# Performance work log

Measured on AMD Instinct MI355X. Metric: run time of the kernel, lower is better.

Reference implementation:

```python
import jax, jax.numpy as jnp
import numpy as np

NEG_INF = -1000000000.0

def setup_inputs() -> dict:
    key = jax.random.key(0)
    k1, k2, k3, k4 = jax.random.split(key, 4)
    N, F_in, F_out, H = 4096, 256, 64, 4
    x = jax.random.normal(k1, (N, F_in), dtype=jnp.float32)
    adj = jax.random.randint(k2, (N, N), 0, 2, dtype=jnp.int32)
    W = jax.random.normal(k3, (H, F_in, F_out), dtype=jnp.float32) * 0.05
    a = jax.random.normal(k4, (H, 2 * F_out, 1), dtype=jnp.float32) * 0.05
    return {"x": x, "adj": adj, "W": W, "a": a}

def reference(x, adj, W, a):
    # x: [N, F_in], adj: [N, N] int, W: [H, F_in, F_out], a: [H, 2*F_out, 1]
    H, F_in, F_out = W.shape
    N = x.shape[0]
    h = jnp.einsum('nf,hfo->hno', x, W)              # [H, N, F_out]
    a1 = a[:, :F_out, 0]                             # [H, F_out] (dot with h_i part of concat)
    a2 = a[:, F_out:, 0]                             # [H, F_out] (dot with h_j part)
    f1 = jnp.einsum('hno,ho->hn', h, a1)             # [H, N]
    f2 = jnp.einsum('hno,ho->hn', h, a2)             # [H, N]
    e = f1[:, :, None] + f2[:, None, :]              # [H, N, N] == dot(concat(h_i,h_j), a)
    e = jnp.where(e >= 0, e, 0.2 * e)                # leaky_relu, slope 0.2
    mask = (adj == 0).astype(jnp.float32) * NEG_INF  # [N, N]
    alpha = jax.nn.softmax(e + mask[None], axis=-1)  # [H, N, N]
    # dropout deterministic (training=False) -> identity
    out = jnp.einsum('hij,hjo->hio', alpha, h)       # [H, N, F_out]
    # concat=True: concat heads along feature dim
    return jnp.transpose(out, (1, 0, 2)).reshape(N, H * F_out)
```

## Files before the change

kernel.cpp:

```cpp
#include <hip/hip_runtime.h>
#include <hip/hip_bf16.h>
#include <stdint.h>

#define LOG2E 1.4426950408889634f

typedef __attribute__((ext_vector_type(4))) float f4;
typedef __attribute__((ext_vector_type(4))) int   i4;
typedef __attribute__((ext_vector_type(8))) short s8;
typedef __attribute__((ext_vector_type(4))) short s4;

#if defined(__has_builtin)
# if __has_builtin(__builtin_amdgcn_exp2f)
#  define EXP2F(x) __builtin_amdgcn_exp2f(x)
# else
#  define EXP2F(x) exp2f(x)
# endif
#else
# define EXP2F(x) exp2f(x)
#endif

static __device__ __forceinline__ uint32_t fbits(float f) {
  union { float f; uint32_t u; } c; c.f = f; return c.u;
}
static __device__ __forceinline__ float ubits(uint32_t u) {
  union { uint32_t u; float f; } c; c.u = u; return c.f;
}
static __device__ __forceinline__ uint16_t bf16_rne(float f) {
  uint32_t b = fbits(f);
  b += 0x7FFFu + ((b >> 16) & 1u);
  return (uint16_t)(b >> 16);
}
static __device__ __forceinline__ float bf2f(uint16_t u) {
  return ubits(((uint32_t)u) << 16);
}
static __device__ __forceinline__ uint32_t fkey(float f) {
  uint32_t u = fbits(f);
  return (u >> 31) ? ~u : (u | 0x80000000u);
}
static __device__ __forceinline__ float unkey(uint32_t k) {
  return ubits((k & 0x80000000u) ? (k ^ 0x80000000u) : ~k);
}

__global__ __launch_bounds__(256) void k_prep_wt(const float* __restrict__ W,
                                                 uint16_t* __restrict__ WT,
                                                 uint32_t* __restrict__ f2mkey) {
  if (blockIdx.x == 0 && threadIdx.x < 4) f2mkey[threadIdx.x] = 0u;
  int idx = (blockIdx.x * 256 + threadIdx.x) * 4;
  f4 w = *(const f4*)(W + idx);
  int h = idx >> 14;
  int k = (idx >> 6) & 255;
  int o = idx & 63;
  uint16_t* base = WT + ((h << 6) + o) * 256 + k;
  base[0]   = bf16_rne(w.x);
  base[256] = bf16_rne(w.y);
  base[512] = bf16_rne(w.z);
  base[768] = bf16_rne(w.w);
}

__global__ __launch_bounds__(256) void k_gemm_h(
    const float* __restrict__ x, const uint16_t* __restrict__ WT,
    const float* __restrict__ a,
    uint16_t* __restrict__ hTf, float* __restrict__ f1, float* __restrict__ f2,
    uint32_t* __restrict__ f2mkey) {
  const int N = 4096, K = 256;
  __shared__ uint16_t xs[16][264];
  int t = threadIdx.x;
  int i0 = blockIdx.x * 16;
  {
    int r = t >> 4, c = (t & 15) << 4;
    const float* src = x + (i0 + r) * K + c;
    union { uint16_t u[16]; s8 v[2]; } tmp;
    #pragma unroll
    for (int i = 0; i < 16; i += 4) {
      f4 v = *(const f4*)(src + i);
      tmp.u[i+0] = bf16_rne(v.x); tmp.u[i+1] = bf16_rne(v.y);
      tmp.u[i+2] = bf16_rne(v.z); tmp.u[i+3] = bf16_rne(v.w);
    }
    *(s8*)&xs[r][c]     = tmp.v[0];
    *(s8*)&xs[r][c + 8] = tmp.v[1];
  }
  __syncthreads();
  int wave = t >> 6, lane = t & 63, lr = lane & 15, lc = lane >> 4;
  f4 acc[4];
  #pragma unroll
  for (int cg = 0; cg < 4; ++cg) acc[cg] = (f4){0.f, 0.f, 0.f, 0.f};
  #pragma unroll
  for (int ks = 0; ks < 8; ++ks) {
    s8 af = *(const s8*)&xs[lr][ks * 32 + lc * 8];
    #pragma unroll
    for (int cg = 0; cg < 4; ++cg) {
      s8 bf = *(const s8*)(WT + ((wave << 6) + (cg << 4) + lr) * 256 + ks * 32 + lc * 8);
      acc[cg] = __builtin_amdgcn_mfma_f32_16x16x32_bf16(af, bf, acc[cg], 0, 0, 0);
    }
  }
  float p1[4] = {0, 0, 0, 0}, p2[4] = {0, 0, 0, 0};
  #pragma unroll
  for (int cg = 0; cg < 4; ++cg) {
    float a1v = a[wave * 128 + (cg << 4) + lr];
    float a2v = a[wave * 128 + 64 + (cg << 4) + lr];
    #pragma unroll
    for (int q = 0; q < 4; ++q) {
      p1[q] = fmaf(acc[cg][q], a1v, p1[q]);
      p2[q] = fmaf(acc[cg][q], a2v, p2[q]);
    }
  }
  #pragma unroll
  for (int m = 1; m <= 8; m <<= 1) {
    #pragma unroll
    for (int q = 0; q < 4; ++q) {
      p1[q] += __shfl_xor(p1[q], m, 64);
      p2[q] += __shfl_xor(p2[q], m, 64);
    }
  }
  if (lr == 0) {
    #pragma unroll
    for (int q = 0; q < 4; ++q) {
      f1[wave * N + i0 + (lc << 2) + q] = p1[q];
      f2[wave * N + i0 + (lc << 2) + q] = p2[q];
    }
  }
  float wm = fmaxf(fmaxf(p2[0], p2[1]), fmaxf(p2[2], p2[3]));
  wm = fmaxf(wm, __shfl_xor(wm, 16, 64));
  wm = fmaxf(wm, __shfl_xor(wm, 32, 64));
  if (lane == 0) atomicMax(&f2mkey[wave], fkey(wm));
  int b0 = (i0 & 31) + (lc << 2);
  int hi = b0 >> 3, e0 = b0 & 7;
  size_t cbase = ((size_t)(wave * 32 + (i0 >> 7)) * 4 + ((i0 >> 5) & 3)) << 2;
  #pragma unroll
  for (int cg = 0; cg < 4; ++cg) {
    union { uint16_t u[4]; s4 v; } h4;
    #pragma unroll
    for (int q = 0; q < 4; ++q) h4.u[q] = bf16_rne(acc[cg][q]);
    *(s4*)(hTf + ((cbase + cg) << 9) + ((hi << 4) + lr) * 8 + e0) = h4.v;
  }
}

__global__ __launch_bounds__(256, 4) void k_attn(
    const int* __restrict__ adj, const float* __restrict__ f1,
    const float* __restrict__ f2, const uint32_t* __restrict__ f2mkey,
    const uint16_t* __restrict__ hTf,
    uint16_t* __restrict__ Op, float* __restrict__ lp, int NP) {
  const int N = 4096;
  __shared__ int adjs[2][32][128];
  int p = blockIdx.x % NP;
  int rb = blockIdx.x / NP;
  int i0 = rb << 5;
  int jcount = N / NP, jbase = p * jcount, ntiles = jcount >> 7;
  int t = threadIdx.x, wave = t >> 6, lane = t & 63, lr = lane & 15, lc = lane >> 4;

  float fm = unkey(f2mkey[wave]);
  float d1[2], d2[2];
  #pragma unroll
  for (int g = 0; g < 2; ++g) {
    float f1v = f1[wave * N + i0 + (g << 4) + lr];
    float s = f1v + fm;
    float M = fmaxf(s, 0.2f * s);
    d1[g] = fmaf(f1v, LOG2E, -M * LOG2E);
    d2[g] = fmaf(f1v, 0.2f * LOG2E, -M * LOG2E);
  }
  f4 acc[2][4], accl[2];
  #pragma unroll
  for (int g = 0; g < 2; ++g) {
    accl[g] = (f4){0.f, 0.f, 0.f, 0.f};
    #pragma unroll
    for (int cg = 0; cg < 4; ++cg) acc[g][cg] = (f4){0.f, 0.f, 0.f, 0.f};
  }
  const s8 ones = {0x3F80, 0x3F80, 0x3F80, 0x3F80, 0x3F80, 0x3F80, 0x3F80, 0x3F80};

  int rloc = (wave << 3) + (lane >> 5);
  int chb = lane & 31;
  const int* gbase = adj + (size_t)(i0 + rloc) * N + jbase;

  #define STAGE(TILE, BUF)                                                    \
    {                                                                         \
      int jc_ = (TILE) << 7;                                                  \
      _Pragma("unroll")                                                       \
      for (int pair = 0; pair < 4; ++pair) {                                  \
        int row_ = rloc + (pair << 1);                                        \
        int ch_ = chb ^ (row_ & 7);           \
        const int* gp_ = gbase + (size_t)(pair << 1) * N + jc_ + (ch_ << 2);  \
        __builtin_amdgcn_global_load_lds(                                     \
            (const __attribute__((address_space(1))) void*)gp_,               \
            (__attribute__((address_space(3))) void*)                         \
                &adjs[BUF][(wave << 3) + (pair << 1)][0],                     \
            16, 0, 0);                                                        \
      }                                                                       \
    }

  const float* f2b = f2 + wave * N + jbase + (lc << 3);
  const uint16_t* hTfb = hTf + (((size_t)(wave * 32) + (jbase >> 7)) << 13) + lane * 8;

  STAGE(0, 0);
  __syncthreads();

  for (int tile = 0;; ++tile) {
    int cur = tile & 1;
    if (tile + 1 < ntiles) STAGE(tile + 1, cur ^ 1);
    const uint16_t* hTft = hTfb + ((size_t)tile << 13);
    #pragma unroll
    for (int ks = 0; ks < 4; ++ks) {
      f4 f2v0 = *(const f4*)(f2b + (tile << 7) + (ks << 5));
      f4 f2v1 = *(const f4*)(f2b + (tile << 7) + (ks << 5) + 4);
      s8 bf[4];
      #pragma unroll
      for (int cg = 0; cg < 4; ++cg)
        bf[cg] = *(const s8*)(hTft + (((ks << 2) + cg) << 9));
      #pragma unroll
      for (int g = 0; g < 2; ++g) {
        const i4* rowp = (const i4*)&adjs[cur][(g << 4) + lr][0];
        int X = (ks << 3) + (lc << 1), s7 = lr & 7;
        i4 a0 = rowp[X ^ s7];
        i4 a1 = rowp[(X + 1) ^ s7];
        uint32_t eb[8];
        #pragma unroll
        for (int e = 0; e < 8; ++e) {
          float f2e = (e < 4) ? f2v0[e] : f2v1[e - 4];
          int   ai  = (e < 4) ? a0[e]   : a1[e - 4];
          float arg = fmaxf(fmaf(f2e, LOG2E, d1[g]),
                            fmaf(f2e, 0.2f * LOG2E, d2[g]));
          eb[e] = (fbits(EXP2F(arg)) & (uint32_t)(-ai)) + 0x8000u;
        }
        union { uint32_t u[4]; s8 v; } af;
        #pragma unroll
        for (int i2 = 0; i2 < 4; ++i2)
          af.u[i2] = __builtin_amdgcn_perm(eb[2 * i2 + 1], eb[2 * i2], 0x07060302u);
        #pragma unroll
        for (int cg = 0; cg < 4; ++cg)
          acc[g][cg] = __builtin_amdgcn_mfma_f32_16x16x32_bf16(af.v, bf[cg],
                                                               acc[g][cg], 0, 0, 0);
        accl[g] = __builtin_amdgcn_mfma_f32_16x16x32_bf16(af.v, ones, accl[g], 0, 0, 0);
      }
    }
    if (tile + 1 >= ntiles) break;
    __syncthreads();
  }
  #undef STAGE

  uint16_t* ob = Op + (size_t)((p << 2) + wave) * N * 64 + (size_t)i0 * 64;
  #pragma unroll
  for (int g = 0; g < 2; ++g) {
    #pragma unroll
    for (int cg = 0; cg < 4; ++cg) {
      #pragma unroll
      for (int q = 0; q < 4; ++q)
        ob[((g << 4) + (lc << 2) + q) * 64 + (cg << 4) + lr] = bf16_rne(acc[g][cg][q]);
    }
    if (lr == 0) {
      #pragma unroll
      for (int q = 0; q < 4; ++q)
        lp[(size_t)((p << 2) + wave) * N + i0 + (g << 4) + (lc << 2) + q] = accl[g][q];
    }
  }
}

__global__ __launch_bounds__(256) void k_combine(
    const uint16_t* __restrict__ Op, const float* __restrict__ lp,
    float* __restrict__ out, int NP) {
  int idx = blockIdx.x * 256 + threadIdx.x;
  int n = idx >> 5;
  int c8 = (idx & 31) << 3;
  int h = c8 >> 6, o = c8 & 63;
  float s[8] = {0, 0, 0, 0, 0, 0, 0, 0};
  float ls = 0.f;
  for (int p = 0; p < NP; ++p) {
    size_t base = (size_t)((p << 2) + h) * 4096 + n;
    s8 v = *(const s8*)(Op + base * 64 + o);
    #pragma unroll
    for (int k = 0; k < 8; ++k) s[k] += bf2f((uint16_t)v[k]);
    ls += lp[base];
  }
  float inv = (ls > 0.f) ? 1.0f / ls : 0.f;
  f4 r0 = {s[0] * inv, s[1] * inv, s[2] * inv, s[3] * inv};
  f4 r1 = {s[4] * inv, s[5] * inv, s[6] * inv, s[7] * inv};
  float* dst = out + (size_t)n * 256 + c8;
  *(f4*)dst = r0;
  *(f4*)(dst + 4) = r1;
}

extern "C" void kernel_launch(void* const* d_in, const int* in_sizes, int n_in,
                              void* d_out, int out_size, void* d_ws, size_t ws_size,
                              hipStream_t stream) {
  (void)in_sizes; (void)n_in; (void)out_size;
  const float* x   = (const float*)d_in[0];
  const int*   adj = (const int*)d_in[1];
  const float* W   = (const float*)d_in[2];
  const float* a   = (const float*)d_in[3];
  float* out = (float*)d_out;
  char* ws = (char*)d_ws;

  size_t oWT = 0;
  size_t oHT = oWT + 131072;
  size_t oF1 = oHT + 2097152;
  size_t oF2 = oF1 + 65536;
  size_t oFM = oF2 + 65536;
  size_t oOP = (oFM + 16 + 255) & ~(size_t)255;

  int NP = 8;
  while (NP > 1 && oOP + (size_t)NP * (2097152 + 65536) > ws_size) NP >>= 1;
  size_t oLP = oOP + (size_t)NP * 2097152;

  uint16_t* WT   = (uint16_t*)(ws + oWT);
  uint16_t* hTf  = (uint16_t*)(ws + oHT);
  float*    f1   = (float*)(ws + oF1);
  float*    f2   = (float*)(ws + oF2);
  uint32_t* f2mk = (uint32_t*)(ws + oFM);
  uint16_t* Op   = (uint16_t*)(ws + oOP);
  float*    lp   = (float*)(ws + oLP);

  k_prep_wt<<<64, 256, 0, stream>>>(W, WT, f2mk);
  k_gemm_h<<<256, 256, 0, stream>>>(x, WT, a, hTf, f1, f2, f2mk);
  k_attn<<<128 * NP, 256, 0, stream>>>(adj, f1, f2, f2mk, hTf, Op, lp, NP);
  k_combine<<<512, 256, 0, stream>>>(Op, lp, out, NP);
}
```

Before: 62.90 us.

## Factor softmax exponent into per-row and per-column exp products in attention

Replaces the per-element exp2 of the leaky-relu score with a product of precomputed per-row factors (exp of f1 terms) and per-column factors (exp of f2 terms, staged in LDS), selecting the branch by comparing the column factor against a per-row threshold. The row-sum is accumulated in VALU from the masked values instead of an extra MFMA against a ones vector. The split count is fixed to 16 with smaller 32-column adjacency tiles, and occupancy is raised to 5 blocks. This removes transcendental work from the inner loop. In exchange it can lose precision or overflow because of the exp products, and it drops the workspace-size fallback.

Result: slower. 104.5 us (+66.2%).

```diff
diff --git a/kernel.cpp b/kernel.cpp
--- a/kernel.cpp
+++ b/kernel.cpp
@@ -2,7 +2,8 @@
 #include <hip/hip_bf16.h>
 #include <stdint.h>
 
-#define LOG2E 1.4426950408889634f
+#define LOG2E  1.4426950408889634f
+#define LOG2E5 0.28853900817779268f
 
 typedef __attribute__((ext_vector_type(4))) float f4;
 typedef __attribute__((ext_vector_type(4))) int   i4;
@@ -135,101 +136,106 @@
   }
 }
 
-__global__ __launch_bounds__(256, 4) void k_attn(
+__global__ __launch_bounds__(256, 5) void k_attn(
     const int* __restrict__ adj, const float* __restrict__ f1,
     const float* __restrict__ f2, const uint32_t* __restrict__ f2mkey,
     const uint16_t* __restrict__ hTf,
-    uint16_t* __restrict__ Op, float* __restrict__ lp, int NP) {
+    uint16_t* __restrict__ Op, float* __restrict__ lp) {
   const int N = 4096;
-  __shared__ int adjs[2][32][128];
-  int p = blockIdx.x % NP;
-  int rb = blockIdx.x / NP;
+  __shared__ int   adjs[2][32][32];
+  __shared__ float E1s[4][256];
+  __shared__ float E2s[4][256];
+  int p  = blockIdx.x & 15;
+  int rb = blockIdx.x >> 4;
   int i0 = rb << 5;
-  int jcount = N / NP, jbase = p * jcount, ntiles = jcount >> 7;
+  int jbase = p << 8;
+  const int ntiles = 8;
   int t = threadIdx.x, wave = t >> 6, lane = t & 63, lr = lane & 15, lc = lane >> 4;
 
   float fm = unkey(f2mkey[wave]);
-  float d1[2], d2[2];
+  float a1f[2], a2f[2], Ti[2], lsum[2] = {0.f, 0.f};
   #pragma unroll
   for (int g = 0; g < 2; ++g) {
     float f1v = f1[wave * N + i0 + (g << 4) + lr];
     float s = f1v + fm;
     float M = fmaxf(s, 0.2f * s);
-    d1[g] = fmaf(f1v, LOG2E, -M * LOG2E);
-    d2[g] = fmaf(f1v, 0.2f * LOG2E, -M * LOG2E);
-  }
-  f4 acc[2][4], accl[2];
-  #pragma unroll
-  for (int g = 0; g < 2; ++g) {
-    accl[g] = (f4){0.f, 0.f, 0.f, 0.f};
+    a1f[g] = EXP2F((f1v - M) * LOG2E);
+    a2f[g] = EXP2F(fmaf(f1v, LOG2E5, -M * LOG2E));
+    Ti[g]  = EXP2F(-f1v * LOG2E);
+  }
+  {
+    int j0 = lane << 2;
+    f4 fv = *(const f4*)(f2 + wave * N + jbase + j0);
+    f4 e1, e2;
+    #pragma unroll
+    for (int k = 0; k < 4; ++k) {
+      e1[k] = EXP2F(fv[k] * LOG2E);
+      e2[k] = EXP2F(fv[k] * LOG2E5);
+    }
+    *(f4*)&E1s[wave][j0] = e1;
+    *(f4*)&E2s[wave][j0] = e2;
+  }
+
+  f4 acc[2][4];
+  #pragma unroll
+  for (int g = 0; g < 2; ++g)
     #pragma unroll
     for (int cg = 0; cg < 4; ++cg) acc[g][cg] = (f4){0.f, 0.f, 0.f, 0.f};
-  }
-  const s8 ones = {0x3F80, 0x3F80, 0x3F80, 0x3F80, 0x3F80, 0x3F80, 0x3F80, 0x3F80};
-
-  int rloc = (wave << 3) + (lane >> 5);
-  int chb = lane & 31;
-  const int* gbase = adj + (size_t)(i0 + rloc) * N + jbase;
-
-  #define STAGE(TILE, BUF)                                                    \
-    {                                                                         \
-      int jc_ = (TILE) << 7;                                                  \
-      _Pragma("unroll")                                                       \
-      for (int pair = 0; pair < 4; ++pair) {                                  \
-        int row_ = rloc + (pair << 1);                                        \
-        int ch_ = chb ^ (row_ & 7);           \
-        const int* gp_ = gbase + (size_t)(pair << 1) * N + jc_ + (ch_ << 2);  \
-        __builtin_amdgcn_global_load_lds(                                     \
-            (const __attribute__((address_space(1))) void*)gp_,               \
-            (__attribute__((address_space(3))) void*)                         \
-                &adjs[BUF][(wave << 3) + (pair << 1)][0],                     \
-            16, 0, 0);                                                        \
-      }                                                                       \
-    }
-
-  const float* f2b = f2 + wave * N + jbase + (lc << 3);
-  const uint16_t* hTfb = hTf + (((size_t)(wave * 32) + (jbase >> 7)) << 13) + lane * 8;
+
+  int srow  = lane >> 3;
+  int sslot = (lane & 7) ^ srow;
+  const int* gbase = adj + (size_t)(i0 + (wave << 3) + srow) * N + jbase + (sslot << 2);
+
+  #define STAGE(TILE, BUF)                                                  \
+    __builtin_amdgcn_global_load_lds(                                       \
+        (const __attribute__((address_space(1))) void*)(gbase + ((TILE) << 5)), \
+        (__attribute__((address_space(3))) void*)&adjs[BUF][wave << 3][0],  \
+        16, 0, 0);
 
   STAGE(0, 0);
   __syncthreads();
+
+  const uint16_t* hTfb = hTf + ((size_t)(wave * 512 + p * 32) << 9) + lane * 8;
 
   for (int tile = 0;; ++tile) {
     int cur = tile & 1;
     if (tile + 1 < ntiles) STAGE(tile + 1, cur ^ 1);
-    const uint16_t* hTft = hTfb + ((size_t)tile << 13);
-    #pragma unroll
-    for (int ks = 0; ks < 4; ++ks) {
-      f4 f2v0 = *(const f4*)(f2b + (tile << 7) + (ks << 5));
-      f4 f2v1 = *(const f4*)(f2b + (tile << 7) + (ks << 5) + 4);
-      s8 bf[4];
+    const uint16_t* hTft = hTfb + ((size_t)tile << 11);
+    s8 bf0 = *(const s8*)(hTft);
+    s8 bf1 = *(const s8*)(hTft + 512);
+    s8 bf2v = *(const s8*)(hTft + 1024);
+    s8 bf3 = *(const s8*)(hTft + 1536);
+    int jo = (tile << 5) + (lc << 3);
+    f4 E1a = *(const f4*)&E1s[wave][jo];
+    f4 E1b = *(const f4*)&E1s[wave][jo + 4];
+    f4 E2a = *(const f4*)&E2s[wave][jo];
+    f4 E2b = *(const f4*)&E2s[wave][jo + 4];
+    #pragma unroll
+    for (int g = 0; g < 2; ++g) {
+      const i4* rowp = (const i4*)&adjs[cur][(g << 4) + lr][0];
+      int sw = lr & 7;
+      i4 a0 = rowp[(lc << 1) ^ sw];
+      i4 a1v = rowp[((lc << 1) + 1) ^ sw];
+      uint32_t eb[8];
       #pragma unroll
-      for (int cg = 0; cg < 4; ++cg)
-        bf[cg] = *(const s8*)(hTft + (((ks << 2) + cg) << 9));
+      for (int e = 0; e < 8; ++e) {
+        float e1 = (e < 4) ? E1a[e] : E1b[e - 4];
+        float e2 = (e < 4) ? E2a[e] : E2b[e - 4];
+        int   ai = (e < 4) ? a0[e]  : a1v[e - 4];
+        bool  c  = e1 >= Ti[g];
+        float pf = (c ? a1f[g] : a2f[g]) * (c ? e1 : e2);
+        uint32_t mb = fbits(pf) & (uint32_t)(-ai);
+        lsum[g] += ubits(mb);
+        eb[e] = mb + 0x8000u;
+      }
+      union { uint32_t u[4]; s8 v; } af;
       #pragma unroll
-      for (int g = 0; g < 2; ++g) {
-        const i4* rowp = (const i4*)&adjs[cur][(g << 4) + lr][0];
-        int X = (ks << 3) + (lc << 1), s7 = lr & 7;
-        i4 a0 = rowp[X ^ s7];
-        i4 a1 = rowp[(X + 1) ^ s7];
-        uint32_t eb[8];
-        #pragma unroll
-        for (int e = 0; e < 8; ++e) {
-          float f2e = (e < 4) ? f2v0[e] : f2v1[e - 4];
-          int   ai  = (e < 4) ? a0[e]   : a1[e - 4];
-          float arg = fmaxf(fmaf(f2e, LOG2E, d1[g]),
-                            fmaf(f2e, 0.2f * LOG2E, d2[g]));
-          eb[e] = (fbits(EXP2F(arg)) & (uint32_t)(-ai)) + 0x8000u;
-        }
-        union { uint32_t u[4]; s8 v; } af;
-        #pragma unroll
-        for (int i2 = 0; i2 < 4; ++i2)
-          af.u[i2] = __builtin_amdgcn_perm(eb[2 * i2 + 1], eb[2 * i2], 0x07060302u);
-        #pragma unroll
-        for (int cg = 0; cg < 4; ++cg)
-          acc[g][cg] = __builtin_amdgcn_mfma_f32_16x16x32_bf16(af.v, bf[cg],
-                                                               acc[g][cg], 0, 0, 0);
-        accl[g] = __builtin_amdgcn_mfma_f32_16x16x32_bf16(af.v, ones, accl[g], 0, 0, 0);
-      }
+      for (int i2 = 0; i2 < 4; ++i2)
+        af.u[i2] = __builtin_amdgcn_perm(eb[2 * i2 + 1], eb[2 * i2], 0x07060302u);
+      acc[g][0] = __builtin_amdgcn_mfma_f32_16x16x32_bf16(af.v, bf0, acc[g][0], 0, 0, 0);
+      acc[g][1] = __builtin_amdgcn_mfma_f32_16x16x32_bf16(af.v, bf1, acc[g][1], 0, 0, 0);
+      acc[g][2] = __builtin_amdgcn_mfma_f32_16x16x32_bf16(af.v, bf2v, acc[g][2], 0, 0, 0);
+      acc[g][3] = __builtin_amdgcn_mfma_f32_16x16x32_bf16(af.v, bf3, acc[g][3], 0, 0, 0);
     }
     if (tile + 1 >= ntiles) break;
     __syncthreads();
@@ -245,11 +251,10 @@
       for (int q = 0; q < 4; ++q)
         ob[((g << 4) + (lc << 2) + q) * 64 + (cg << 4) + lr] = bf16_rne(acc[g][cg][q]);
     }
-    if (lr == 0) {
-      #pragma unroll
-      for (int q = 0; q < 4; ++q)
-        lp[(size_t)((p << 2) + wave) * N + i0 + (g << 4) + (lc << 2) + q] = accl[g][q];
-    }
+    float v = lsum[g];
+    v += __shfl_xor(v, 16, 64);
+    v += __shfl_xor(v, 32, 64);
+    if (lane < 16) lp[(size_t)((p << 2) + wave) * N + i0 + (g << 4) + lane] = v;
   }
 }
 
@@ -280,7 +285,7 @@
 extern "C" void kernel_launch(void* const* d_in, const int* in_sizes, int n_in,
                               void* d_out, int out_size, void* d_ws, size_t ws_size,
                               hipStream_t stream) {
-  (void)in_sizes; (void)n_in; (void)out_size;
+  (void)in_sizes; (void)n_in; (void)out_size; (void)ws_size;
   const float* x   = (const float*)d_in[0];
   const int*   adj = (const int*)d_in[1];
   const float* W   = (const float*)d_in[2];
@@ -288,15 +293,13 @@
   float* out = (float*)d_out;
   char* ws = (char*)d_ws;
 
+  const int NP = 16;
   size_t oWT = 0;
   size_t oHT = oWT + 131072;
   size_t oF1 = oHT + 2097152;
   size_t oF2 = oF1 + 65536;
   size_t oFM = oF2 + 65536;
   size_t oOP = (oFM + 16 + 255) & ~(size_t)255;
-
-  int NP = 8;
-  while (NP > 1 && oOP + (size_t)NP * (2097152 + 65536) > ws_size) NP >>= 1;
   size_t oLP = oOP + (size_t)NP * 2097152;
 
   uint16_t* WT   = (uint16_t*)(ws + oWT);
@@ -309,6 +312,6 @@
 
   k_prep_wt<<<64, 256, 0, stream>>>(W, WT, f2mk);
   k_gemm_h<<<256, 256, 0, stream>>>(x, WT, a, hTf, f1, f2, f2mk);
-  k_attn<<<128 * NP, 256, 0, stream>>>(adj, f1, f2, f2mk, hTf, Op, lp, NP);
+  k_attn<<<128 * NP, 256, 0, stream>>>(adj, f1, f2, f2mk, hTf, Op, lp);
   k_combine<<<512, 256, 0, stream>>>(Op, lp, out, NP);
 }
```

## Pack adjacency into transposed bitmask and read bits directly in attention kernel

Applied to the files above, without the earlier changes.

A new pre-pass kernel uses wave ballots to compress the int32 adjacency matrix into a transposed 1-bit-per-entry mask. The attention kernel then reads mask words straight from global memory, so the LDS staging, double buffering and block barriers are gone. The j-split is fixed at 16 partitions, which doubles the partial-output traffic the combine kernel must reduce and drops the workspace-size fallback. The full 64 MB adjacency is still read once by the pack kernel, which adds one launch.

Result: slower. 77.45 us (+23.1%).

```diff
diff --git a/kernel.cpp b/kernel.cpp
--- a/kernel.cpp
+++ b/kernel.cpp
@@ -2,7 +2,8 @@
 #include <hip/hip_bf16.h>
 #include <stdint.h>
 
-#define LOG2E 1.4426950408889634f
+#define LOG2E  1.4426950408889634f
+#define LOG2E5 0.28853900817779268f
 
 typedef __attribute__((ext_vector_type(4))) float f4;
 typedef __attribute__((ext_vector_type(4))) int   i4;
@@ -39,6 +40,19 @@
 }
 static __device__ __forceinline__ float unkey(uint32_t k) {
   return ubits((k & 0x80000000u) ? (k ^ 0x80000000u) : ~k);
+}
+
+__global__ __launch_bounds__(256) void k_pack(const int* __restrict__ adj,
+                                              uint32_t* __restrict__ bitsT) {
+  int gw = (blockIdx.x * 256 + threadIdx.x) >> 6;
+  int lane = threadIdx.x & 63;
+  for (int task = gw; task < 262144; task += 8192) {
+    int r = task >> 6, cp = task & 63;
+    int v = adj[((size_t)r << 12) + (cp << 6) + lane];
+    uint64_t b = __ballot(v != 0);
+    if (lane == 0)  bitsT[(size_t)(cp * 2 + 0) * 4096 + r] = (uint32_t)b;
+    if (lane == 32) bitsT[(size_t)(cp * 2 + 1) * 4096 + r] = (uint32_t)(b >> 32);
+  }
 }
 
 __global__ __launch_bounds__(256) void k_prep_wt(const float* __restrict__ W,
@@ -136,16 +150,15 @@
 }
 
 __global__ __launch_bounds__(256, 4) void k_attn(
-    const int* __restrict__ adj, const float* __restrict__ f1,
+    const uint32_t* __restrict__ bitsT, const float* __restrict__ f1,
     const float* __restrict__ f2, const uint32_t* __restrict__ f2mkey,
     const uint16_t* __restrict__ hTf,
-    uint16_t* __restrict__ Op, float* __restrict__ lp, int NP) {
+    uint16_t* __restrict__ Op, float* __restrict__ lp) {
   const int N = 4096;
-  __shared__ int adjs[2][32][128];
-  int p = blockIdx.x % NP;
-  int rb = blockIdx.x / NP;
+  int p  = blockIdx.x & 15;
+  int rb = blockIdx.x >> 4;
   int i0 = rb << 5;
-  int jcount = N / NP, jbase = p * jcount, ntiles = jcount >> 7;
+  int jbase = p << 8;
   int t = threadIdx.x, wave = t >> 6, lane = t & 63, lr = lane & 15, lc = lane >> 4;
 
   float fm = unkey(f2mkey[wave]);
@@ -156,7 +169,7 @@
     float s = f1v + fm;
     float M = fmaxf(s, 0.2f * s);
     d1[g] = fmaf(f1v, LOG2E, -M * LOG2E);
-    d2[g] = fmaf(f1v, 0.2f * LOG2E, -M * LOG2E);
+    d2[g] = fmaf(f1v, LOG2E5, -M * LOG2E);
   }
   f4 acc[2][4], accl[2];
   #pragma unroll
@@ -167,74 +180,44 @@
   }
   const s8 ones = {0x3F80, 0x3F80, 0x3F80, 0x3F80, 0x3F80, 0x3F80, 0x3F80, 0x3F80};
 
-  int rloc = (wave << 3) + (lane >> 5);
-  int chb = lane & 31;
-  const int* gbase = adj + (size_t)(i0 + rloc) * N + jbase;
-
-  #define STAGE(TILE, BUF)                                                    \
-    {                                                                         \
-      int jc_ = (TILE) << 7;                                                  \
-      _Pragma("unroll")                                                       \
-      for (int pair = 0; pair < 4; ++pair) {                                  \
-        int row_ = rloc + (pair << 1);                                        \
-        int ch_ = chb ^ (row_ & 7);           \
-        const int* gp_ = gbase + (size_t)(pair << 1) * N + jc_ + (ch_ << 2);  \
-        __builtin_amdgcn_global_load_lds(                                     \
-            (const __attribute__((address_space(1))) void*)gp_,               \
-            (__attribute__((address_space(3))) void*)                         \
-                &adjs[BUF][(wave << 3) + (pair << 1)][0],                     \
-            16, 0, 0);                                                        \
-      }                                                                       \
-    }
-
+  const uint32_t* bwp = bitsT + ((size_t)(p << 3) << 12) + i0 + lr;
   const float* f2b = f2 + wave * N + jbase + (lc << 3);
-  const uint16_t* hTfb = hTf + (((size_t)(wave * 32) + (jbase >> 7)) << 13) + lane * 8;
-
-  STAGE(0, 0);
-  __syncthreads();
-
-  for (int tile = 0;; ++tile) {
-    int cur = tile & 1;
-    if (tile + 1 < ntiles) STAGE(tile + 1, cur ^ 1);
-    const uint16_t* hTft = hTfb + ((size_t)tile << 13);
-    #pragma unroll
-    for (int ks = 0; ks < 4; ++ks) {
-      f4 f2v0 = *(const f4*)(f2b + (tile << 7) + (ks << 5));
-      f4 f2v1 = *(const f4*)(f2b + (tile << 7) + (ks << 5) + 4);
-      s8 bf[4];
-      #pragma unroll
-      for (int cg = 0; cg < 4; ++cg)
-        bf[cg] = *(const s8*)(hTft + (((ks << 2) + cg) << 9));
-      #pragma unroll
-      for (int g = 0; g < 2; ++g) {
-        const i4* rowp = (const i4*)&adjs[cur][(g << 4) + lr][0];
-        int X = (ks << 3) + (lc << 1), s7 = lr & 7;
-        i4 a0 = rowp[X ^ s7];
-        i4 a1 = rowp[(X + 1) ^ s7];
-        uint32_t eb[8];
-        #pragma unroll
-        for (int e = 0; e < 8; ++e) {
-          float f2e = (e < 4) ? f2v0[e] : f2v1[e - 4];
-          int   ai  = (e < 4) ? a0[e]   : a1[e - 4];
-          float arg = fmaxf(fmaf(f2e, LOG2E, d1[g]),
-                            fmaf(f2e, 0.2f * LOG2E, d2[g]));
-          eb[e] = (fbits(EXP2F(arg)) & (uint32_t)(-ai)) + 0x8000u;
-        }
-        union { uint32_t u[4]; s8 v; } af;
-        #pragma unroll
-        for (int i2 = 0; i2 < 4; ++i2)
-          af.u[i2] = __builtin_amdgcn_perm(eb[2 * i2 + 1], eb[2 * i2], 0x07060302u);
-        #pragma unroll
-        for (int cg = 0; cg < 4; ++cg)
-          acc[g][cg] = __builtin_amdgcn_mfma_f32_16x16x32_bf16(af.v, bf[cg],
-                                                               acc[g][cg], 0, 0, 0);
-        accl[g] = __builtin_amdgcn_mfma_f32_16x16x32_bf16(af.v, ones, accl[g], 0, 0, 0);
+  const uint16_t* hTfb = hTf + ((size_t)(wave * 512 + p * 32) << 9) + lane * 8;
+  int sh = lc << 3;
+
+  #pragma unroll
+  for (int c = 0; c < 8; ++c) {
+    uint32_t ws0 = bwp[c << 12] >> sh;
+    uint32_t ws1 = bwp[(c << 12) + 16] >> sh;
+    f4 f2v0 = *(const f4*)(f2b + (c << 5));
+    f4 f2v1 = *(const f4*)(f2b + (c << 5) + 4);
+    s8 bf0 = *(const s8*)(hTfb + ((c << 2) << 9));
+    s8 bf1 = *(const s8*)(hTfb + (((c << 2) + 1) << 9));
+    s8 bf2v = *(const s8*)(hTfb + (((c << 2) + 2) << 9));
+    s8 bf3 = *(const s8*)(hTfb + (((c << 2) + 3) << 9));
+    #pragma unroll
+    for (int g = 0; g < 2; ++g) {
+      uint32_t ws = g ? ws1 : ws0;
+      uint32_t eb[8];
+      #pragma unroll
+      for (int e = 0; e < 8; ++e) {
+        float f2e = (e < 4) ? f2v0[e] : f2v1[e - 4];
+        float arg = fmaxf(fmaf(f2e, LOG2E, d1[g]),
+                          fmaf(f2e, LOG2E5, d2[g]));
+        uint32_t msk = 0u - ((ws >> e) & 1u);
+        eb[e] = (fbits(EXP2F(arg)) & msk) + 0x8000u;
       }
-    }
-    if (tile + 1 >= ntiles) break;
-    __syncthreads();
-  }
-  #undef STAGE
+      union { uint32_t u[4]; s8 v; } af;
+      #pragma unroll
+      for (int i2 = 0; i2 < 4; ++i2)
+        af.u[i2] = __builtin_amdgcn_perm(eb[2 * i2 + 1], eb[2 * i2], 0x07060302u);
+      acc[g][0] = __builtin_amdgcn_mfma_f32_16x16x32_bf16(af.v, bf0, acc[g][0], 0, 0, 0);
+      acc[g][1] = __builtin_amdgcn_mfma_f32_16x16x32_bf16(af.v, bf1, acc[g][1], 0, 0, 0);
+      acc[g][2] = __builtin_amdgcn_mfma_f32_16x16x32_bf16(af.v, bf2v, acc[g][2], 0, 0, 0);
+      acc[g][3] = __builtin_amdgcn_mfma_f32_16x16x32_bf16(af.v, bf3, acc[g][3], 0, 0, 0);
+      accl[g]   = __builtin_amdgcn_mfma_f32_16x16x32_bf16(af.v, ones, accl[g], 0, 0, 0);
+    }
+  }
 
   uint16_t* ob = Op + (size_t)((p << 2) + wave) * N * 64 + (size_t)i0 * 64;
   #pragma unroll
@@ -280,7 +263,7 @@
 extern "C" void kernel_launch(void* const* d_in, const int* in_sizes, int n_in,
                               void* d_out, int out_size, void* d_ws, size_t ws_size,
                               hipStream_t stream) {
-  (void)in_sizes; (void)n_in; (void)out_size;
+  (void)in_sizes; (void)n_in; (void)out_size; (void)ws_size;
   const float* x   = (const float*)d_in[0];
   const int*   adj = (const int*)d_in[1];
   const float* W   = (const float*)d_in[2];
@@ -288,27 +271,28 @@
   float* out = (float*)d_out;
   char* ws = (char*)d_ws;
 
+  const int NP = 16;
   size_t oWT = 0;
   size_t oHT = oWT + 131072;
   size_t oF1 = oHT + 2097152;
   size_t oF2 = oF1 + 65536;
   size_t oFM = oF2 + 65536;
-  size_t oOP = (oFM + 16 + 255) & ~(size_t)255;
-
-  int NP = 8;
-  while (NP > 1 && oOP + (size_t)NP * (2097152 + 65536) > ws_size) NP >>= 1;
+  size_t oBT = (oFM + 16 + 255) & ~(size_t)255;
+  size_t oOP = oBT + 2097152;
   size_t oLP = oOP + (size_t)NP * 2097152;
 
-  uint16_t* WT   = (uint16_t*)(ws + oWT);
-  uint16_t* hTf  = (uint16_t*)(ws + oHT);
-  float*    f1   = (float*)(ws + oF1);
-  float*    f2   = (float*)(ws + oF2);
-  uint32_t* f2mk = (uint32_t*)(ws + oFM);
-  uint16_t* Op   = (uint16_t*)(ws + oOP);
-  float*    lp   = (float*)(ws + oLP);
-
+  uint16_t* WT    = (uint16_t*)(ws + oWT);
+  uint16_t* hTf   = (uint16_t*)(ws + oHT);
+  float*    f1    = (float*)(ws + oF1);
+  float*    f2    = (float*)(ws + oF2);
+  uint32_t* f2mk  = (uint32_t*)(ws + oFM);
+  uint32_t* bitsT = (uint32_t*)(ws + oBT);
+  uint16_t* Op    = (uint16_t*)(ws + oOP);
+  float*    lp    = (float*)(ws + oLP);
+
+  k_pack<<<2048, 256, 0, stream>>>(adj, bitsT);
   k_prep_wt<<<64, 256, 0, stream>>>(W, WT, f2mk);
   k_gemm_h<<<256, 256, 0, stream>>>(x, WT, a, hTf, f1, f2, f2mk);
-  k_attn<<<128 * NP, 256, 0, stream>>>(adj, f1, f2, f2mk, hTf, Op, lp, NP);
+  k_attn<<<128 * NP, 256, 0, stream>>>(bitsT, f1, f2, f2mk, hTf, Op, lp);
   k_combine<<<512, 256, 0, stream>>>(Op, lp, out, NP);
 }
```
